# Optimization experiments

Measured on AMD Instinct MI355X. Metric: run time of the kernel, lower is better.

## Reference

```python
import jax, jax.numpy as jnp
import numpy as np
from jax import lax

# ---- static config (matches init_kwargs) ----
STRIDE = 16
BASE_SIZE = 16
SCALES = np.array([2., 4., 8., 16., 32.])
RATIOS = np.array([0.5, 1., 2.])
CLIP = 4.14
NMS_THRESH = 0.7
PRE_NMS = 6000
POST_NMS = 300
MIN_SIZE = 16.0


def _whctrs(a):
    w = a[2] - a[0] + 1.0
    h = a[3] - a[1] + 1.0
    return w, h, a[0] + 0.5 * (w - 1.0), a[1] + 0.5 * (h - 1.0)


def _mkanchors(ws, hs, xc, yc):
    return np.stack([xc - 0.5 * (ws - 1.0), yc - 0.5 * (hs - 1.0),
                     xc + 0.5 * (ws - 1.0), yc + 0.5 * (hs - 1.0)], axis=1)


def _base_anchors():
    ba = np.array([1.0, 1.0, BASE_SIZE, BASE_SIZE]) - 1.0
    w, h, xc, yc = _whctrs(ba)
    size = w * h
    ws = np.round(np.sqrt(size / RATIOS))
    hs = np.round(ws * RATIOS)
    ra = _mkanchors(ws, hs, xc, yc)
    out = []
    for i in range(ra.shape[0]):
        w, h, xc, yc = _whctrs(ra[i])
        out.append(_mkanchors(w * SCALES, h * SCALES, xc, yc))
    return np.concatenate(out, axis=0)  # (A,4), A = len(ratios)*len(scales)


def _grid_anchors(Hf, Wf):
    ba = _base_anchors()                       # (A,4)
    sx, sy = np.meshgrid(np.arange(Wf) * STRIDE, np.arange(Hf) * STRIDE)
    shifts = np.stack([sx, sy, sx, sy], axis=-1)          # (Hf,Wf,4)
    anch = shifts[:, :, None, :] + ba[None, None, :, :]    # (Hf,Wf,A,4)
    return jnp.asarray(anch.reshape(1, -1, 4), dtype=jnp.float32)


def _decode_clip(anchors, deltas, img_h, img_w):
    # NormalizedBoxCenterDecoder (stds=1) + clip to image
    aw = anchors[..., 2] - anchors[..., 0]
    ah = anchors[..., 3] - anchors[..., 1]
    ax = anchors[..., 0] + 0.5 * aw
    ay = anchors[..., 1] + 0.5 * ah
    dx, dy, dw, dh = deltas[..., 0], deltas[..., 1], deltas[..., 2], deltas[..., 3]
    ox = dx * aw + ax
    oy = dy * ah + ay
    ow = jnp.exp(jnp.minimum(dw, CLIP)) * aw * 0.5
    oh = jnp.exp(jnp.minimum(dh, CLIP)) * ah * 0.5
    x1 = jnp.clip(ox - ow, 0.0, img_w - 1.0)
    y1 = jnp.clip(oy - oh, 0.0, img_h - 1.0)
    x2 = jnp.clip(ox + ow, 0.0, img_w - 1.0)
    y2 = jnp.clip(oy + oh, 0.0, img_h - 1.0)
    return jnp.stack([x1, y1, x2, y2], axis=-1)


def _nms_single(scores, boxes):
    # scores (N,), boxes (N,4). Greedy NMS, force_suppress, sorted by score desc.
    order = jnp.argsort(-scores)[:PRE_NMS]
    s = scores[order]
    b = boxes[order]
    x1, y1, x2, y2 = b[:, 0], b[:, 1], b[:, 2], b[:, 3]
    area = (x2 - x1) * (y2 - y1)
    iw = jnp.maximum(jnp.minimum(x2[:, None], x2[None, :]) - jnp.maximum(x1[:, None], x1[None, :]), 0.0)
    ih = jnp.maximum(jnp.minimum(y2[:, None], y2[None, :]) - jnp.maximum(y1[:, None], y1[None, :]), 0.0)
    inter = iw * ih
    iou = inter / (area[:, None] + area[None, :] - inter + 1e-12)  # (PRE,PRE)

    supp0 = s < 0.0  # invalid entries (score set to -1 by min_size filter)

    def body(supp, i):
        keep = jnp.logical_not(supp[i])
        new = jnp.where(keep, jnp.logical_or(supp, iou[i] > NMS_THRESH), supp)
        new = new.at[i].set(supp[i])  # never self-suppress
        return new, None

    supp, _ = lax.scan(body, supp0, jnp.arange(PRE_NMS))
    kept = jnp.logical_not(supp)
    perm = jnp.argsort(jnp.where(kept, 0, 1), stable=True)  # kept boxes first, order preserved
    out_s = jnp.where(kept[perm], s[perm], -1.0)
    out_b = jnp.where(kept[perm][:, None], b[perm], -1.0)
    return out_s[:POST_NMS, None], out_b[:POST_NMS]


def _forward(img, x, conv_w, conv_b, score_w, score_b, loc_w, loc_b):
    B, _, Hf, Wf = x.shape
    img_h, img_w = float(img.shape[2]), float(img.shape[3])
    anchors = _grid_anchors(Hf, Wf)  # (1, Hf*Wf*A, 4)

    # conv1 3x3 pad 1 + ReLU
    h = lax.conv_general_dilated(x, conv_w, (1, 1), [(1, 1), (1, 1)],
                                 dimension_numbers=('NCHW', 'OIHW', 'NCHW'))
    h = jax.nn.relu(h + conv_b[None, :, None, None])

    A = score_w.shape[0]
    raw_scores = jnp.einsum('bchw,oc->bhwo', h, score_w.reshape(A, -1)) + score_b
    raw_scores = raw_scores.reshape(B, -1, 1)                       # (B,N,1)
    raw_boxes = jnp.einsum('bchw,oc->bhwo', h, loc_w.reshape(4 * A, -1)) + loc_b
    raw_boxes = raw_boxes.reshape(B, -1, 4)                         # (B,N,4)

    rpn_scores = jax.nn.sigmoid(raw_scores)

    roi = _decode_clip(anchors, raw_boxes, img_h, img_w)            # (B,N,4)
    width = roi[..., 2] - roi[..., 0]
    height = roi[..., 3] - roi[..., 1]
    invalid = jnp.logical_or(width < MIN_SIZE, height < MIN_SIZE)   # (B,N)
    score = jnp.where(invalid[..., None], -1.0, rpn_scores)         # (B,N,1)
    roi = jnp.where(invalid[..., None], -1.0, roi)

    out_s, out_b = jax.vmap(_nms_single)(score[..., 0], roi)        # (B,300,1),(B,300,4)
    return jnp.concatenate([out_s, out_b], axis=-1)                 # (B,300,5)


def setup_inputs() -> dict:
    key = jax.random.key(0)
    ks = jax.random.split(key, 8)
    img = jax.random.normal(ks[0], (1, 3, 1024, 1024), jnp.float32)
    x = jax.random.normal(ks[1], (1, 1024, 64, 64), jnp.float32)
    conv_w = jax.random.normal(ks[2], (1024, 1024, 3, 3), jnp.float32) * 0.01
    conv_b = jnp.zeros((1024,), jnp.float32)
    score_w = jax.random.normal(ks[3], (15, 1024, 1, 1), jnp.float32) * 0.01
    score_b = jnp.zeros((15,), jnp.float32)
    loc_w = jax.random.normal(ks[4], (60, 1024, 1, 1), jnp.float32) * 0.002
    loc_b = jnp.zeros((60,), jnp.float32)
    return {"img": img, "x": x, "conv_w": conv_w, "conv_b": conv_b,
            "score_w": score_w, "score_b": score_b, "loc_w": loc_w, "loc_b": loc_b}


def reference(img, x, conv_w, conv_b, score_w, score_b, loc_w, loc_b):
    return _forward(img, x, conv_w, conv_b, score_w, score_b, loc_w, loc_b)
```

## Files before the change

kernel.cpp:

```cpp
#include <hip/hip_runtime.h>

typedef unsigned int uint;
typedef unsigned short ushort;
typedef unsigned long long u64;

typedef __attribute__((ext_vector_type(8))) short short8;
typedef __attribute__((ext_vector_type(4))) float floatx4;

__device__ inline ushort bf16rne(float v) {
  uint b = __float_as_uint(v);
  uint r = (b + 0x7fffu + ((b >> 16) & 1u)) >> 16;
  return (ushort)r;
}

__device__ inline void gl_lds16(const void* g, void* l) {
  __builtin_amdgcn_global_load_lds(
      (const __attribute__((address_space(1))) unsigned int*)g,
      (__attribute__((address_space(3))) unsigned int*)l, 16, 0, 0);
}


__global__ __launch_bounds__(256) void prep_x(const float* __restrict__ x,
                                              ushort* __restrict__ xh,
                                              ushort* __restrict__ xl) {
  __shared__ float tile[8][512];
  int cc = blockIdx.x, sg = blockIdx.y, t = threadIdx.x;
  int ci0 = cc * 32 + sg * 8;
  size_t obase = (size_t)(cc * 4 + sg) * 4356;
  for (int it = 0; it < 4; ++it) {
    int s0 = blockIdx.z * 2048 + it * 512;
#pragma unroll
    for (int e = 0; e < 8; ++e) {
      tile[e][t] = x[(size_t)(ci0 + e) * 4096 + s0 + t];
      tile[e][t + 256] = x[(size_t)(ci0 + e) * 4096 + s0 + 256 + t];
    }
    __syncthreads();
#pragma unroll
    for (int w = 0; w < 2; ++w) {
      int sl = w * 256 + t;
      int s = s0 + sl;
      int y = s >> 6, xx = s & 63;
      short8 sh, slo;
#pragma unroll
      for (int e = 0; e < 8; ++e) {
        float v = tile[e][sl];
        ushort h2 = bf16rne(v);
        float hf = __uint_as_float((uint)h2 << 16);
        sh[e] = (short)h2;
        slo[e] = (short)bf16rne(v - hf);
      }
      size_t o = (obase + (size_t)(y + 1) * 66 + (xx + 1)) * 8;
      *(short8*)(xh + o) = sh;
      *(short8*)(xl + o) = slo;
    }
    __syncthreads();
  }
}

__global__ __launch_bounds__(256) void prep_w(const float* __restrict__ w,
                                              ushort* __restrict__ wh,
                                              ushort* __restrict__ wl) {
  int cc = blockIdx.x, sg = blockIdx.y, t = threadIdx.x;
  int e = t & 7, col = t >> 3;
  int ci = cc * 32 + sg * 8 + e;
  for (int chunk = 0; chunk < 8; ++chunk) {
    int co = blockIdx.z * 256 + chunk * 32 + col;
    const float* src = w + ((size_t)co * 1024 + ci) * 9;
    float v[9];
#pragma unroll
    for (int o = 0; o < 9; ++o) v[o] = src[o];
#pragma unroll
    for (int off = 0; off < 9; ++off) {
      ushort h2 = bf16rne(v[off]);
      float hf = __uint_as_float((uint)h2 << 16);
      ushort l2 = bf16rne(v[off] - hf);
      size_t oi = ((size_t)(off * 32 + cc) * 4 + sg) * 8192 + (size_t)co * 8 + e;
      wh[oi] = h2;
      wl[oi] = l2;
    }
  }
}

__global__ __launch_bounds__(256) void prep_head(
    const float* __restrict__ score_w, const float* __restrict__ loc_w,
    const float* __restrict__ score_b, const float* __restrict__ loc_b,
    ushort* __restrict__ wh, ushort* __restrict__ wl, float* __restrict__ bh) {
  int idx = blockIdx.x * 256 + threadIdx.x;
  int o = idx >> 10, ci = idx & 1023;
  float v = 0.f;
  if (o < 15) v = score_w[o * 1024 + ci];
  else if (o < 75) v = loc_w[(o - 15) * 1024 + ci];
  ushort h2 = bf16rne(v);
  float hf = __uint_as_float((uint)h2 << 16);
  int cc = ci >> 5, sg = (ci >> 3) & 3, e = ci & 7;
  size_t oi = ((size_t)(cc * 4 + sg) * 128 + o) * 8 + e;
  wh[oi] = h2;
  wl[oi] = bf16rne(v - hf);
  if (idx < 128) bh[idx] = (idx < 15) ? score_b[idx] : ((idx < 75) ? loc_b[idx - 15] : 0.f);
}

__global__ __launch_bounds__(256, 1) void gemm_conv(
    const ushort* __restrict__ Ahi, const ushort* __restrict__ Alo,
    const ushort* __restrict__ Bhi, const ushort* __restrict__ Blo,
    const float* __restrict__ bias, ushort* __restrict__ outHi,
    ushort* __restrict__ outLo) {
  constexpr int NC = 288;
  constexpr int ASEC = 128 * 32;
  constexpr int BSEC = 64 * 32;
  constexpr int BUFU = 2 * ASEC + 2 * BSEC;
  __shared__ ushort sm[2 * BUFU];
  const int t = threadIdx.x;
  const int m0 = blockIdx.x * 128;
  const int n0 = blockIdx.y * 64;

  const int lane = t & 63, wv = t >> 6;
  const int wm = (wv & 1) * 64, wn = (wv >> 1) * 32;
  const int rA = wm + (lane & 15);
  const int rB = wn + (lane & 15);
  const int segA = (lane >> 4) * 2048;
  const int segB = (lane >> 4) * 1024;

  auto stage = [&](int c, int bufIdx) {
    ushort* secAh = sm + bufIdx * BUFU;
    ushort* secAl = secAh + ASEC;
    ushort* secBh = secAl + ASEC;
    ushort* secBl = secBh + BSEC;
    int off = c >> 5, cc = c & 31;
    int oy = off / 3, ox = off - 3 * oy;
#pragma unroll
    for (int q = 0; q < 2; ++q) {
      int L = t + 256 * q;
      int row = L & 127, seg = L >> 7;
      int m = m0 + row, y = m >> 6, xq = m & 63;
      size_t aoff = ((size_t)(cc * 4 + seg) * 4356 + (y + oy) * 66 + (xq + ox)) * 16;
      gl_lds16((const char*)Ahi + aoff, (char*)secAh + L * 16);
      gl_lds16((const char*)Alo + aoff, (char*)secAl + L * 16);
    }
    {
      int L = t;
      int row = L & 63, seg = L >> 6;
      size_t boff = (((size_t)(off * 32 + cc) * 4 + seg) * 1024 + (n0 + row)) * 16;
      gl_lds16((const char*)Bhi + boff, (char*)secBh + L * 16);
      gl_lds16((const char*)Blo + boff, (char*)secBl + L * 16);
    }
  };

  floatx4 acc[4][2];
#pragma unroll
  for (int i = 0; i < 4; ++i)
#pragma unroll
    for (int j = 0; j < 2; ++j) acc[i][j] = (floatx4){0.f, 0.f, 0.f, 0.f};

  auto compute = [&](const ushort* sb) {
    const char* cAh = (const char*)sb;
    const char* cAl = (const char*)(sb + ASEC);
    const char* cBh = (const char*)(sb + 2 * ASEC);
    const char* cBl = (const char*)(sb + 2 * ASEC + BSEC);
    short8 ah[4], al[4], bh2[2], bl2[2];
#pragma unroll
    for (int i = 0; i < 4; ++i) {
      int pa = segA + (rA + 16 * i) * 16;
      ah[i] = *(const short8*)(cAh + pa);
      al[i] = *(const short8*)(cAl + pa);
    }
#pragma unroll
    for (int j = 0; j < 2; ++j) {
      int pb = segB + (rB + 16 * j) * 16;
      bh2[j] = *(const short8*)(cBh + pb);
      bl2[j] = *(const short8*)(cBl + pb);
    }
#pragma unroll
    for (int i = 0; i < 4; ++i)
#pragma unroll
      for (int j = 0; j < 2; ++j) {
        acc[i][j] = __builtin_amdgcn_mfma_f32_16x16x32_bf16(ah[i], bh2[j], acc[i][j], 0, 0, 0);
        acc[i][j] = __builtin_amdgcn_mfma_f32_16x16x32_bf16(ah[i], bl2[j], acc[i][j], 0, 0, 0);
        acc[i][j] = __builtin_amdgcn_mfma_f32_16x16x32_bf16(al[i], bh2[j], acc[i][j], 0, 0, 0);
      }
  };

  stage(0, 0);
  for (int kc = 0; kc < NC; ++kc) {
    __syncthreads();
    if (kc + 1 < NC) stage(kc + 1, (kc + 1) & 1);
    compute(sm + (kc & 1) * BUFU);
  }

#pragma unroll
  for (int i = 0; i < 4; ++i)
#pragma unroll
    for (int j = 0; j < 2; ++j) {
      int nn = n0 + wn + 16 * j + (lane & 15);
      float bv = bias[nn];
#pragma unroll
      for (int r = 0; r < 4; ++r) {
        int mm = m0 + wm + 16 * i + (lane >> 4) * 4 + r;
        float v = fmaxf(acc[i][j][r] + bv, 0.f);
        ushort h2 = bf16rne(v);
        float hf = __uint_as_float((uint)h2 << 16);
        ushort l2 = bf16rne(v - hf);
        int cc = nn >> 5, sg = (nn >> 3) & 3, e = nn & 7;
        size_t ho = ((size_t)(cc * 4 + sg) * 4096 + mm) * 8 + e;
        outHi[ho] = h2;
        outLo[ho] = l2;
      }
    }
}

template <int BM, int BN>
__global__ __launch_bounds__(256, 1) void gemm_head(
    const ushort* __restrict__ Ahi, const ushort* __restrict__ Alo,
    const ushort* __restrict__ Bhi, const ushort* __restrict__ Blo,
    const float* __restrict__ bias, int nChunks, float* __restrict__ outRaw) {
  constexpr int ASEC = BM * 32;
  constexpr int BUFU = 2 * ASEC;
  constexpr int WM = (BM >= 128) ? 2 : 1;
  constexpr int WN = 4 / WM;
  constexpr int MI = (BM / WM) / 16;
  constexpr int NJ = (BN / WN) / 16;
  __shared__ ushort sm[2 * BUFU];
  const int t = threadIdx.x;
  const int m0 = blockIdx.x * BM;
  const int n0 = blockIdx.y * BN;

  const int lane = t & 63, wv = t >> 6;
  const int wm = (wv % WM) * (BM / WM);
  const int wn = (wv / WM) * (BN / WN);
  const int rA = wm + (lane & 15);
  const int segA = (lane >> 4) * (BM * 16);

  auto stage = [&](int c, int bufIdx) {
    ushort* secAh = sm + bufIdx * BUFU;
    ushort* secAl = secAh + ASEC;
    for (int L = t; L < BM * 4; L += 256) {
      int row = L % BM, seg = L / BM;
      size_t aoff = ((size_t)(c * 4 + seg) * 4096 + (m0 + row)) * 16;
      gl_lds16((const char*)Ahi + aoff, (char*)secAh + L * 16);
      gl_lds16((const char*)Alo + aoff, (char*)secAl + L * 16);
    }
  };

  auto loadB = [&](int c, short8* bh, short8* bl) {
    int sg = lane >> 4;
#pragma unroll
    for (int j = 0; j < NJ; ++j) {
      int co = n0 + wn + (lane & 15) + 16 * j;
      size_t boff = (((size_t)(c * 4 + sg)) * 128 + co) * 16;
      bh[j] = *(const short8*)((const char*)Bhi + boff);
      bl[j] = *(const short8*)((const char*)Blo + boff);
    }
  };

  floatx4 acc[MI][NJ];
#pragma unroll
  for (int i = 0; i < MI; ++i)
#pragma unroll
    for (int j = 0; j < NJ; ++j) acc[i][j] = (floatx4){0.f, 0.f, 0.f, 0.f};

  auto compute = [&](const ushort* sb, const short8* bh2, const short8* bl2) {
    const char* cAh = (const char*)sb;
    const char* cAl = (const char*)(sb + ASEC);
    short8 ah[MI], al[MI];
#pragma unroll
    for (int i = 0; i < MI; ++i) {
      int pa = segA + (rA + 16 * i) * 16;
      ah[i] = *(const short8*)(cAh + pa);
      al[i] = *(const short8*)(cAl + pa);
    }
#pragma unroll
    for (int i = 0; i < MI; ++i)
#pragma unroll
      for (int j = 0; j < NJ; ++j) {
        acc[i][j] = __builtin_amdgcn_mfma_f32_16x16x32_bf16(ah[i], bh2[j], acc[i][j], 0, 0, 0);
        acc[i][j] = __builtin_amdgcn_mfma_f32_16x16x32_bf16(ah[i], bl2[j], acc[i][j], 0, 0, 0);
        acc[i][j] = __builtin_amdgcn_mfma_f32_16x16x32_bf16(al[i], bh2[j], acc[i][j], 0, 0, 0);
      }
  };

  short8 b0h[NJ], b0l[NJ], b1h[NJ], b1l[NJ];
  stage(0, 0);
  loadB(0, b0h, b0l);
  for (int kc = 0; kc < nChunks; kc += 2) {
    __syncthreads();
    if (kc + 1 < nChunks) { stage(kc + 1, 1); loadB(kc + 1, b1h, b1l); }
    compute(sm, b0h, b0l);
    __syncthreads();
    if (kc + 2 < nChunks) { stage(kc + 2, 0); loadB(kc + 2, b0h, b0l); }
    compute(sm + BUFU, b1h, b1l);
  }

#pragma unroll
  for (int i = 0; i < MI; ++i)
#pragma unroll
    for (int j = 0; j < NJ; ++j) {
      int nn = n0 + wn + 16 * j + (lane & 15);
      float bv = bias[nn];
#pragma unroll
      for (int r = 0; r < 4; ++r) {
        int mm = m0 + wm + 16 * i + (lane >> 4) * 4 + r;
        outRaw[(size_t)mm * 128 + nn] = acc[i][j][r] + bv;
      }
    }
}

__global__ __launch_bounds__(256) void decode_k(const float* __restrict__ raw,
                                                float* __restrict__ scores,
                                                float4* __restrict__ boxes,
                                                uint* __restrict__ key32,
                                                uint* __restrict__ hist) {
  int i = blockIdx.x * 256 + threadIdx.x;
  int m = i / 15, a = i - m * 15;
  int y = m >> 6, x = m & 63;
  const float* rp = raw + (size_t)m * 128;
  float logit = rp[a];
  float dx = rp[15 + 4 * a], dy = rp[16 + 4 * a];
  float dw = rp[17 + 4 * a], dh = rp[18 + 4 * a];
  int rr = a / 5, ss = a - rr * 5;
  float sc5 = (float)(2 << ss);
  float W = ((rr == 0) ? 23.f : (rr == 1) ? 16.f : 11.f) * sc5;
  float H = ((rr == 0) ? 12.f : (rr == 1) ? 16.f : 22.f) * sc5;
  float aw = W - 1.f, ah = H - 1.f;
  float ax = x * 16.f + 7.5f, ay = y * 16.f + 7.5f;
  float ox = dx * aw + ax, oyc = dy * ah + ay;
  float ow = expf(fminf(dw, 4.14f)) * aw * 0.5f;
  float oh = expf(fminf(dh, 4.14f)) * ah * 0.5f;
  float x1 = fminf(fmaxf(ox - ow, 0.f), 1023.f);
  float y1 = fminf(fmaxf(oyc - oh, 0.f), 1023.f);
  float x2 = fminf(fmaxf(ox + ow, 0.f), 1023.f);
  float y2 = fminf(fmaxf(oyc + oh, 0.f), 1023.f);
  bool inval = ((x2 - x1) < 16.f) || ((y2 - y1) < 16.f);
  float sc = inval ? -1.f : (1.f / (1.f + expf(-logit)));
  scores[i] = sc;
  boxes[i] = inval ? make_float4(-1.f, -1.f, -1.f, -1.f) : make_float4(x1, y1, x2, y2);
  uint kb = __float_as_uint(sc);
  uint key = (kb & 0x80000000u) ? ~kb : (kb | 0x80000000u);
  key32[i] = key;
  atomicAdd(&hist[key >> 16], 1u);
}

__global__ __launch_bounds__(256) void seg_sum(const uint* __restrict__ hist,
                                               uint* __restrict__ segsum) {
  __shared__ uint red[256];
  int b = blockIdx.x, t = threadIdx.x;
  red[t] = hist[b * 256 + t];
  __syncthreads();
  for (int d = 128; d > 0; d >>= 1) {
    if (t < d) red[t] += red[t + d];
    __syncthreads();
  }
  if (t == 0) segsum[b] = red[0];
}

__global__ __launch_bounds__(256) void find_t16(const uint* __restrict__ hist,
                                                const uint* __restrict__ segsum,
                                                uint* __restrict__ selT) {
  __shared__ uint ps[256];
  __shared__ int segS;
  int t = threadIdx.x;
  ps[t] = segsum[t];
  __syncthreads();
  for (int d = 1; d < 256; d <<= 1) {
    uint v = ps[t] + ((t + d < 256) ? ps[t + d] : 0u);
    __syncthreads();
    ps[t] = v;
    __syncthreads();
  }
  if (ps[t] >= 6000u && (t == 255 || ps[t + 1] < 6000u)) segS = t;
  __syncthreads();
  int sg = segS;
  uint base = (sg == 255) ? 0u : ps[sg + 1];
  uint h2 = hist[sg * 256 + t];
  __syncthreads();
  ps[t] = h2;
  __syncthreads();
  for (int d = 1; d < 256; d <<= 1) {
    uint v = ps[t] + ((t + d < 256) ? ps[t + d] : 0u);
    __syncthreads();
    ps[t] = v;
    __syncthreads();
  }
  if (base + ps[t] >= 6000u && (t == 255 || base + ps[t + 1] < 6000u))
    *selT = (uint)(sg * 256 + t);
}

__global__ __launch_bounds__(256) void gather_k(const uint* __restrict__ key32,
                                                const uint* __restrict__ selT,
                                                uint* __restrict__ cnt,
                                                u64* __restrict__ cand) {
  int i = blockIdx.x * 256 + threadIdx.x;
  uint T = *selT;
  uint k = key32[i];
  if ((k >> 16) >= T) {
    uint pos = atomicAdd(cnt, 1u);
    if (pos < 8192) cand[pos] = ((u64)k << 32) | (u64)(~(uint)i);
  }
}

__global__ __launch_bounds__(1024) void sort_gather(
    const u64* __restrict__ cand, const uint* __restrict__ cnt,
    const float* __restrict__ scores, const float4* __restrict__ boxes,
    float* __restrict__ sortedS, float4* __restrict__ sortedB) {
  extern __shared__ u64 sk[];
  int t = threadIdx.x;
  int C = (int)*cnt;
  if (C > 8192) C = 8192;
  for (int j = t; j < 8192; j += 1024) sk[j] = (j < C) ? cand[j] : 0ull;
  __syncthreads();
  for (int k = 2; k <= 8192; k <<= 1) {
    for (int j2 = k >> 1; j2 > 0; j2 >>= 1) {
      for (int p = t; p < 4096; p += 1024) {
        int i = ((p & ~(j2 - 1)) << 1) | (p & (j2 - 1));
        int ix = i | j2;
        u64 a = sk[i], b = sk[ix];
        bool ddir = (i & k) != 0;
        if ((a < b) != ddir) { sk[i] = b; sk[ix] = a; }
      }
      __syncthreads();
    }
  }
  for (int j = t; j < 6016; j += 1024) {
    if (j < 6000) {
      u64 key = sk[j];
      uint idx = ~(uint)(key & 0xffffffffu);
      sortedS[j] = scores[idx];
      sortedB[j] = boxes[idx];
    } else {
      sortedS[j] = -1.f;
      sortedB[j] = make_float4(0.f, 0.f, 0.f, 0.f);
    }
  }
}

__global__ __launch_bounds__(64) void iou_mask(const float4* __restrict__ boxes,
                                               u64* __restrict__ mask) {
  __shared__ float cx1[64], cy1[64], cx2[64], cy2[64], car[64];
  int bi = blockIdx.x, bj = blockIdx.y, t = threadIdx.x;
  float4 cb = boxes[bj * 64 + t];
  cx1[t] = cb.x; cy1[t] = cb.y; cx2[t] = cb.z; cy2[t] = cb.w;
  car[t] = (cb.z - cb.x) * (cb.w - cb.y);
  __syncthreads();
  int r = bi * 64 + t;
  float4 rb = boxes[r];
  float ra = (rb.z - rb.x) * (rb.w - rb.y);
  u64 wd = 0;
#pragma unroll 8
  for (int j = 0; j < 64; ++j) {
    float iw = fmaxf(fminf(rb.z, cx2[j]) - fmaxf(rb.x, cx1[j]), 0.f);
    float ih = fmaxf(fminf(rb.w, cy2[j]) - fmaxf(rb.y, cy1[j]), 0.f);
    float inter = iw * ih;
    float iou = inter / (ra + car[j] - inter + 1e-12f);
    if (iou > 0.7f && r != bj * 64 + j) wd |= (1ull << j);
  }
  mask[(size_t)r * 128 + bj] = wd;
}

__global__ __launch_bounds__(64) void nms_scan(const u64* __restrict__ mask,
                                               const float* __restrict__ sortedS,
                                               const float4* __restrict__ sortedB,
                                               float* __restrict__ out) {
  __shared__ int klist[300];
  int lane = threadIdx.x;
  u64 Sx = 0, Sy = 0;
  for (int w2 = 0; w2 < 94; ++w2) {
    bool neg = sortedS[w2 * 64 + lane] < 0.f;
    u64 m2 = __ballot(neg);
    if ((w2 >> 1) == lane) { if (w2 & 1) Sy = m2; else Sx = m2; }
  }
  int count = 0;
  for (int w2 = 0; w2 < 94; ++w2) {
    u64 cur = __shfl((w2 & 1) ? Sy : Sx, w2 >> 1);
    u64 rem = ~cur;
    if (w2 == 93) rem &= (1ull << 48) - 1;
    if (!rem) continue;
    int bA = __builtin_ctzll(rem);
    ulonglong2 vA = ((const ulonglong2*)(mask + (size_t)(w2 * 64 + bA) * 128))[lane];
    int bB;
    ulonglong2 vB;
    for (;;) {
      {
        u64 remS = (bA == 63) ? 0ull : (rem & (~0ull << (bA + 1)));
        bB = remS ? __builtin_ctzll(remS) : -1;
        if (bB >= 0)
          vB = ((const ulonglong2*)(mask + (size_t)(w2 * 64 + bB) * 128))[lane];
        if (lane == 0) klist[count] = w2 * 64 + bA;
        count++;
        if (count == 300) goto done;
        Sx |= vA.x;
        Sy |= vA.y;
        u64 cur2 = __shfl((w2 & 1) ? Sy : Sx, w2 >> 1);
        rem = remS & ~cur2;
        if (!rem) break;
        int bn = __builtin_ctzll(rem);
        if (bn != bB) {
          bB = bn;
          vB = ((const ulonglong2*)(mask + (size_t)(w2 * 64 + bB) * 128))[lane];
        }
      }
      {
        u64 remS = (bB == 63) ? 0ull : (rem & (~0ull << (bB + 1)));
        bA = remS ? __builtin_ctzll(remS) : -1;
        if (bA >= 0)
          vA = ((const ulonglong2*)(mask + (size_t)(w2 * 64 + bA) * 128))[lane];
        if (lane == 0) klist[count] = w2 * 64 + bB;
        count++;
        if (count == 300) goto done;
        Sx |= vB.x;
        Sy |= vB.y;
        u64 cur2 = __shfl((w2 & 1) ? Sy : Sx, w2 >> 1);
        rem = remS & ~cur2;
        if (!rem) break;
        int bn = __builtin_ctzll(rem);
        if (bn != bA) {
          bA = bn;
          vA = ((const ulonglong2*)(mask + (size_t)(w2 * 64 + bA) * 128))[lane];
        }
      }
    }
  }
done:
  __syncthreads();
  for (int j = lane; j < 300; j += 64) {
    float s;
    float4 bb;
    if (j < count) {
      int i = klist[j];
      s = sortedS[i];
      bb = sortedB[i];
    } else {
      s = -1.f;
      bb = make_float4(-1.f, -1.f, -1.f, -1.f);
    }
    out[j * 5 + 0] = s;
    out[j * 5 + 1] = bb.x;
    out[j * 5 + 2] = bb.y;
    out[j * 5 + 3] = bb.z;
    out[j * 5 + 4] = bb.w;
  }
}

constexpr size_t O_XH = 0;
constexpr size_t O_XL = 8921088;
constexpr size_t O_WTH = 17842176;
constexpr size_t O_WTL = 36716544;
constexpr size_t O_HH = 55590912;
constexpr size_t O_HL = 63979520;
constexpr size_t O_WHH = 72368128;
constexpr size_t O_WHL = 72630272;
constexpr size_t O_BHD = 72892416;
constexpr size_t O_SC = 72892928;
constexpr size_t O_BX = 73138688;
constexpr size_t O_KEY = 74121728;
constexpr size_t O_HIST = 74367488;
constexpr size_t O_CNT = 74629632;
constexpr size_t O_CAND = 74629888;
constexpr size_t O_SELT = 74695424;
constexpr size_t O_SS = 74695680;
constexpr size_t O_SB = 74719744;
constexpr size_t O_RAW = 0;
constexpr size_t O_MASK = 17842176;
constexpr size_t O_SEG = 24002560;

extern "C" void kernel_launch(void* const* d_in, const int* in_sizes, int n_in,
                              void* d_out, int out_size, void* d_ws,
                              size_t ws_size, hipStream_t stream) {
  (void)in_sizes; (void)n_in; (void)out_size; (void)ws_size;
  const float* x = (const float*)d_in[1];
  const float* conv_w = (const float*)d_in[2];
  const float* conv_b = (const float*)d_in[3];
  const float* score_w = (const float*)d_in[4];
  const float* score_b = (const float*)d_in[5];
  const float* loc_w = (const float*)d_in[6];
  const float* loc_b = (const float*)d_in[7];
  float* out = (float*)d_out;
  char* ws = (char*)d_ws;

  ushort* xh = (ushort*)(ws + O_XH);
  ushort* xl = (ushort*)(ws + O_XL);
  ushort* wTh = (ushort*)(ws + O_WTH);
  ushort* wTl = (ushort*)(ws + O_WTL);
  ushort* hh = (ushort*)(ws + O_HH);
  ushort* hl = (ushort*)(ws + O_HL);
  ushort* wHh = (ushort*)(ws + O_WHH);
  ushort* wHl = (ushort*)(ws + O_WHL);
  float* biasH = (float*)(ws + O_BHD);
  float* raw = (float*)(ws + O_RAW);
  float* scores = (float*)(ws + O_SC);
  float4* boxes = (float4*)(ws + O_BX);
  uint* key32 = (uint*)(ws + O_KEY);
  uint* hist = (uint*)(ws + O_HIST);
  uint* cnt = (uint*)(ws + O_CNT);
  u64* cand = (u64*)(ws + O_CAND);
  uint* selT = (uint*)(ws + O_SELT);
  float* sortedS = (float*)(ws + O_SS);
  float4* sortedB = (float4*)(ws + O_SB);
  u64* mask = (u64*)(ws + O_MASK);
  uint* segsum = (uint*)(ws + O_SEG);

  hipMemsetAsync(ws + O_XH, 0, 2 * 8921088, stream);
  hipMemsetAsync(ws + O_HIST, 0, 262144 + 256, stream);

  prep_x<<<dim3(32, 4, 2), 256, 0, stream>>>(x, xh, xl);
  prep_w<<<dim3(32, 4, 4), 256, 0, stream>>>(conv_w, wTh, wTl);
  prep_head<<<512, 256, 0, stream>>>(score_w, loc_w, score_b, loc_b, wHh, wHl, biasH);

  gemm_conv<<<dim3(32, 16), 256, 0, stream>>>(xh, xl, wTh, wTl, conv_b, hh, hl);
  gemm_head<32, 128><<<dim3(128, 1), 256, 0, stream>>>(hh, hl, wHh, wHl, biasH,
                                                       32, raw);

  decode_k<<<240, 256, 0, stream>>>(raw, scores, boxes, key32, hist);
  seg_sum<<<256, 256, 0, stream>>>(hist, segsum);
  find_t16<<<1, 256, 0, stream>>>(hist, segsum, selT);
  gather_k<<<240, 256, 0, stream>>>(key32, selT, cnt, cand);
  sort_gather<<<1, 1024, 65536, stream>>>(cand, cnt, scores, boxes, sortedS, sortedB);
  iou_mask<<<dim3(94, 94), 64, 0, stream>>>(sortedB, mask);
  nms_scan<<<1, 64, 0, stream>>>(mask, sortedS, sortedB, out);
}
```

Before: 707.8 us.

## Fuse head GEMM with box decode and restructure NMS scan per word

The head GEMM now stages its 32x128 output tile in shared memory and decodes anchors, scores, keys and histogram entries in the same kernel, which removes the raw buffer round-trip and one kernel launch. The NMS scan is rewritten to resolve suppression within each 64-candidate word using the diagonal mask word and warp shuffles, then OR the kept rows' masks in with a small prefetch queue, in place of the serial dependent row loads. This adds shared memory use in the GEMM kernel and adds code complexity to the scan.

```diff
diff --git a/kernel.cpp b/kernel.cpp
--- a/kernel.cpp
+++ b/kernel.cpp
@@ -207,26 +207,24 @@
     }
 }
 
-template <int BM, int BN>
-__global__ __launch_bounds__(256, 1) void gemm_head(
+__global__ __launch_bounds__(256, 1) void gemm_head_decode(
     const ushort* __restrict__ Ahi, const ushort* __restrict__ Alo,
     const ushort* __restrict__ Bhi, const ushort* __restrict__ Blo,
-    const float* __restrict__ bias, int nChunks, float* __restrict__ outRaw) {
+    const float* __restrict__ bias, float* __restrict__ scores,
+    float4* __restrict__ boxes, uint* __restrict__ key32,
+    uint* __restrict__ hist) {
+  constexpr int BM = 32, BN = 128, NCH = 32;
   constexpr int ASEC = BM * 32;
   constexpr int BUFU = 2 * ASEC;
-  constexpr int WM = (BM >= 128) ? 2 : 1;
-  constexpr int WN = 4 / WM;
-  constexpr int MI = (BM / WM) / 16;
-  constexpr int NJ = (BN / WN) / 16;
+  constexpr int MI = 2, NJ = 2;
   __shared__ ushort sm[2 * BUFU];
+  __shared__ float rawT[32][128];
   const int t = threadIdx.x;
   const int m0 = blockIdx.x * BM;
-  const int n0 = blockIdx.y * BN;
 
   const int lane = t & 63, wv = t >> 6;
-  const int wm = (wv % WM) * (BM / WM);
-  const int wn = (wv / WM) * (BN / WN);
-  const int rA = wm + (lane & 15);
+  const int wn = wv * 32;
+  const int rA = lane & 15;
   const int segA = (lane >> 4) * (BM * 16);
 
   auto stage = [&](int c, int bufIdx) {
@@ -244,7 +242,7 @@
     int sg = lane >> 4;
 #pragma unroll
     for (int j = 0; j < NJ; ++j) {
-      int co = n0 + wn + (lane & 15) + 16 * j;
+      int co = wn + (lane & 15) + 16 * j;
       size_t boff = (((size_t)(c * 4 + sg)) * 128 + co) * 16;
       bh[j] = *(const short8*)((const char*)Bhi + boff);
       bl[j] = *(const short8*)((const char*)Blo + boff);
@@ -280,62 +278,64 @@
   short8 b0h[NJ], b0l[NJ], b1h[NJ], b1l[NJ];
   stage(0, 0);
   loadB(0, b0h, b0l);
-  for (int kc = 0; kc < nChunks; kc += 2) {
-    __syncthreads();
-    if (kc + 1 < nChunks) { stage(kc + 1, 1); loadB(kc + 1, b1h, b1l); }
+  for (int kc = 0; kc < NCH; kc += 2) {
+    __syncthreads();
+    if (kc + 1 < NCH) { stage(kc + 1, 1); loadB(kc + 1, b1h, b1l); }
     compute(sm, b0h, b0l);
     __syncthreads();
-    if (kc + 2 < nChunks) { stage(kc + 2, 0); loadB(kc + 2, b0h, b0l); }
+    if (kc + 2 < NCH) { stage(kc + 2, 0); loadB(kc + 2, b0h, b0l); }
     compute(sm + BUFU, b1h, b1l);
   }
 
+  __syncthreads();
 #pragma unroll
   for (int i = 0; i < MI; ++i)
 #pragma unroll
     for (int j = 0; j < NJ; ++j) {
-      int nn = n0 + wn + 16 * j + (lane & 15);
+      int nn = wn + 16 * j + (lane & 15);
       float bv = bias[nn];
 #pragma unroll
       for (int r = 0; r < 4; ++r) {
-        int mm = m0 + wm + 16 * i + (lane >> 4) * 4 + r;
-        outRaw[(size_t)mm * 128 + nn] = acc[i][j][r] + bv;
+        int lm = 16 * i + (lane >> 4) * 4 + r;
+        rawT[lm][nn] = acc[i][j][r] + bv;
       }
     }
-}
-
-__global__ __launch_bounds__(256) void decode_k(const float* __restrict__ raw,
-                                                float* __restrict__ scores,
-                                                float4* __restrict__ boxes,
-                                                uint* __restrict__ key32,
-                                                uint* __restrict__ hist) {
-  int i = blockIdx.x * 256 + threadIdx.x;
-  int m = i / 15, a = i - m * 15;
-  int y = m >> 6, x = m & 63;
-  const float* rp = raw + (size_t)m * 128;
-  float logit = rp[a];
-  float dx = rp[15 + 4 * a], dy = rp[16 + 4 * a];
-  float dw = rp[17 + 4 * a], dh = rp[18 + 4 * a];
-  int rr = a / 5, ss = a - rr * 5;
-  float sc5 = (float)(2 << ss);
-  float W = ((rr == 0) ? 23.f : (rr == 1) ? 16.f : 11.f) * sc5;
-  float H = ((rr == 0) ? 12.f : (rr == 1) ? 16.f : 22.f) * sc5;
-  float aw = W - 1.f, ah = H - 1.f;
-  float ax = x * 16.f + 7.5f, ay = y * 16.f + 7.5f;
-  float ox = dx * aw + ax, oyc = dy * ah + ay;
-  float ow = expf(fminf(dw, 4.14f)) * aw * 0.5f;
-  float oh = expf(fminf(dh, 4.14f)) * ah * 0.5f;
-  float x1 = fminf(fmaxf(ox - ow, 0.f), 1023.f);
-  float y1 = fminf(fmaxf(oyc - oh, 0.f), 1023.f);
-  float x2 = fminf(fmaxf(ox + ow, 0.f), 1023.f);
-  float y2 = fminf(fmaxf(oyc + oh, 0.f), 1023.f);
-  bool inval = ((x2 - x1) < 16.f) || ((y2 - y1) < 16.f);
-  float sc = inval ? -1.f : (1.f / (1.f + expf(-logit)));
-  scores[i] = sc;
-  boxes[i] = inval ? make_float4(-1.f, -1.f, -1.f, -1.f) : make_float4(x1, y1, x2, y2);
-  uint kb = __float_as_uint(sc);
-  uint key = (kb & 0x80000000u) ? ~kb : (kb | 0x80000000u);
-  key32[i] = key;
-  atomicAdd(&hist[key >> 16], 1u);
+  __syncthreads();
+
+#pragma unroll
+  for (int it = 0; it < 2; ++it) {
+    int item = it * 256 + t;
+    if (item >= 480) break;
+    int lm = item / 15, a = item - lm * 15;
+    int m = m0 + lm;
+    int i = m * 15 + a;
+    int y = m >> 6, x = m & 63;
+    const float* rp = &rawT[lm][0];
+    float logit = rp[a];
+    float dx = rp[15 + 4 * a], dy = rp[16 + 4 * a];
+    float dw = rp[17 + 4 * a], dh = rp[18 + 4 * a];
+    int rr = a / 5, ss = a - rr * 5;
+    float sc5 = (float)(2 << ss);
+    float W = ((rr == 0) ? 23.f : (rr == 1) ? 16.f : 11.f) * sc5;
+    float H = ((rr == 0) ? 12.f : (rr == 1) ? 16.f : 22.f) * sc5;
+    float aw = W - 1.f, ah = H - 1.f;
+    float ax = x * 16.f + 7.5f, ay = y * 16.f + 7.5f;
+    float ox = dx * aw + ax, oyc = dy * ah + ay;
+    float ow = expf(fminf(dw, 4.14f)) * aw * 0.5f;
+    float oh = expf(fminf(dh, 4.14f)) * ah * 0.5f;
+    float x1 = fminf(fmaxf(ox - ow, 0.f), 1023.f);
+    float y1 = fminf(fmaxf(oyc - oh, 0.f), 1023.f);
+    float x2 = fminf(fmaxf(ox + ow, 0.f), 1023.f);
+    float y2 = fminf(fmaxf(oyc + oh, 0.f), 1023.f);
+    bool inval = ((x2 - x1) < 16.f) || ((y2 - y1) < 16.f);
+    float sc = inval ? -1.f : (1.f / (1.f + expf(-logit)));
+    scores[i] = sc;
+    boxes[i] = inval ? make_float4(-1.f, -1.f, -1.f, -1.f) : make_float4(x1, y1, x2, y2);
+    uint kb = __float_as_uint(sc);
+    uint key = (kb & 0x80000000u) ? ~kb : (kb | 0x80000000u);
+    key32[i] = key;
+    atomicAdd(&hist[key >> 16], 1u);
+  }
 }
 
 __global__ __launch_bounds__(256) void seg_sum(const uint* __restrict__ hist,
@@ -467,57 +467,57 @@
     if ((w2 >> 1) == lane) { if (w2 & 1) Sy = m2; else Sx = m2; }
   }
   int count = 0;
-  for (int w2 = 0; w2 < 94; ++w2) {
+  for (int w2 = 0; w2 < 94 && count < 300; ++w2) {
     u64 cur = __shfl((w2 & 1) ? Sy : Sx, w2 >> 1);
     u64 rem = ~cur;
     if (w2 == 93) rem &= (1ull << 48) - 1;
     if (!rem) continue;
-    int bA = __builtin_ctzll(rem);
-    ulonglong2 vA = ((const ulonglong2*)(mask + (size_t)(w2 * 64 + bA) * 128))[lane];
-    int bB;
-    ulonglong2 vB;
-    for (;;) {
-      {
-        u64 remS = (bA == 63) ? 0ull : (rem & (~0ull << (bA + 1)));
-        bB = remS ? __builtin_ctzll(remS) : -1;
-        if (bB >= 0)
-          vB = ((const ulonglong2*)(mask + (size_t)(w2 * 64 + bB) * 128))[lane];
-        if (lane == 0) klist[count] = w2 * 64 + bA;
-        count++;
-        if (count == 300) goto done;
-        Sx |= vA.x;
-        Sy |= vA.y;
-        u64 cur2 = __shfl((w2 & 1) ? Sy : Sx, w2 >> 1);
-        rem = remS & ~cur2;
-        if (!rem) break;
-        int bn = __builtin_ctzll(rem);
-        if (bn != bB) {
-          bB = bn;
-          vB = ((const ulonglong2*)(mask + (size_t)(w2 * 64 + bB) * 128))[lane];
-        }
+    u64 W = 0;
+    if ((rem >> lane) & 1)
+      W = mask[(size_t)(w2 * 64 + lane) * 128 + w2];
+    u64 acc = 0, live = rem;
+    bool full = false;
+    while (live) {
+      int b = __builtin_ctzll(live);
+      acc |= 1ull << b;
+      ++count;
+      if (count == 300) { full = true; break; }
+      u64 wb = __shfl(W, b);
+      live &= ~wb;
+      live &= (b == 63) ? 0ull : (~0ull << (b + 1));
+    }
+    if (lane == 0) {
+      u64 a2 = acc;
+      int idx = count - __builtin_popcountll(acc);
+      while (a2) {
+        int b = __builtin_ctzll(a2);
+        klist[idx++] = w2 * 64 + b;
+        a2 &= a2 - 1;
       }
-      {
-        u64 remS = (bB == 63) ? 0ull : (rem & (~0ull << (bB + 1)));
-        bA = remS ? __builtin_ctzll(remS) : -1;
-        if (bA >= 0)
-          vA = ((const ulonglong2*)(mask + (size_t)(w2 * 64 + bA) * 128))[lane];
-        if (lane == 0) klist[count] = w2 * 64 + bB;
-        count++;
-        if (count == 300) goto done;
-        Sx |= vB.x;
-        Sy |= vB.y;
-        u64 cur2 = __shfl((w2 & 1) ? Sy : Sx, w2 >> 1);
-        rem = remS & ~cur2;
-        if (!rem) break;
-        int bn = __builtin_ctzll(rem);
-        if (bn != bA) {
-          bA = bn;
-          vA = ((const ulonglong2*)(mask + (size_t)(w2 * 64 + bA) * 128))[lane];
-        }
-      }
-    }
-  }
-done:
+    }
+    if (full) break;
+    u64 a2 = acc;
+    int r0 = -1, r1 = -1, r2 = -1, r3 = -1;
+    ulonglong2 v0, v1, v2, v3;
+    if (a2) { int b = __builtin_ctzll(a2); a2 &= a2 - 1; r0 = w2 * 64 + b;
+      v0 = ((const ulonglong2*)(mask + (size_t)r0 * 128))[lane]; }
+    if (a2) { int b = __builtin_ctzll(a2); a2 &= a2 - 1; r1 = w2 * 64 + b;
+      v1 = ((const ulonglong2*)(mask + (size_t)r1 * 128))[lane]; }
+    if (a2) { int b = __builtin_ctzll(a2); a2 &= a2 - 1; r2 = w2 * 64 + b;
+      v2 = ((const ulonglong2*)(mask + (size_t)r2 * 128))[lane]; }
+    if (a2) { int b = __builtin_ctzll(a2); a2 &= a2 - 1; r3 = w2 * 64 + b;
+      v3 = ((const ulonglong2*)(mask + (size_t)r3 * 128))[lane]; }
+    while (r0 >= 0) {
+      Sx |= v0.x;
+      Sy |= v0.y;
+      r0 = r1; v0 = v1;
+      r1 = r2; v1 = v2;
+      r2 = r3; v2 = v3;
+      r3 = -1;
+      if (a2) { int b = __builtin_ctzll(a2); a2 &= a2 - 1; r3 = w2 * 64 + b;
+        v3 = ((const ulonglong2*)(mask + (size_t)r3 * 128))[lane]; }
+    }
+  }
   __syncthreads();
   for (int j = lane; j < 300; j += 64) {
     float s;
@@ -556,7 +556,6 @@
 constexpr size_t O_SELT = 74695424;
 constexpr size_t O_SS = 74695680;
 constexpr size_t O_SB = 74719744;
-constexpr size_t O_RAW = 0;
 constexpr size_t O_MASK = 17842176;
 constexpr size_t O_SEG = 24002560;
 
@@ -583,7 +582,6 @@
   ushort* wHh = (ushort*)(ws + O_WHH);
   ushort* wHl = (ushort*)(ws + O_WHL);
   float* biasH = (float*)(ws + O_BHD);
-  float* raw = (float*)(ws + O_RAW);
   float* scores = (float*)(ws + O_SC);
   float4* boxes = (float4*)(ws + O_BX);
   uint* key32 = (uint*)(ws + O_KEY);
@@ -604,10 +602,9 @@
   prep_head<<<512, 256, 0, stream>>>(score_w, loc_w, score_b, loc_b, wHh, wHl, biasH);
 
   gemm_conv<<<dim3(32, 16), 256, 0, stream>>>(xh, xl, wTh, wTl, conv_b, hh, hl);
-  gemm_head<32, 128><<<dim3(128, 1), 256, 0, stream>>>(hh, hl, wHh, wHl, biasH,
-                                                       32, raw);
-
-  decode_k<<<240, 256, 0, stream>>>(raw, scores, boxes, key32, hist);
+  gemm_head_decode<<<dim3(128, 1), 256, 0, stream>>>(hh, hl, wHh, wHl, biasH,
+                                                     scores, boxes, key32, hist);
+
   seg_sum<<<256, 256, 0, stream>>>(hist, segsum);
   find_t16<<<1, 256, 0, stream>>>(hist, segsum, selT);
   gather_k<<<240, 256, 0, stream>>>(key32, selT, cnt, cand);
```

New measurement: 699.5 us. Within noise of the previous version (-1.2%).
